# Optimization experiments

Hardware: AMD Instinct MI355X
Metric: run time of the kernel (lower is better)

Reference implementation:

```python
import jax, jax.numpy as jnp
import numpy as np

DIMENSIONS = 10000
NUM_LEVELS = 256
SIZE = 28
BATCH = 64
NUM_CLASSES = 10


def _bipolar(key, shape):
    # torchhd MAP hypervectors are random +/-1
    return jnp.where(jax.random.uniform(key, shape) > 0.5, 1.0, -1.0).astype(jnp.float32)


def setup_inputs() -> dict:
    key = jax.random.key(0)
    kx, kpx, kpy, kv, kw = jax.random.split(key, 5)
    # pixel intensities in [0, 1]
    x = jax.random.uniform(kx, (BATCH, SIZE, SIZE), dtype=jnp.float32)
    # position = hard_quantize(bundle(px, py)) with px, py random bipolar HVs
    px = _bipolar(kpx, (SIZE * SIZE, DIMENSIONS))
    py = _bipolar(kpy, (SIZE * SIZE, DIMENSIONS))
    position = jnp.where(px + py > 0, 1.0, -1.0).astype(jnp.float32)
    # Level embedding table (bipolar hypervectors per intensity level)
    level_weight = _bipolar(kv, (NUM_LEVELS, DIMENSIONS))
    # classify Linear weight (zero in original; small random here so output is non-trivial)
    classify_weight = jax.random.normal(kw, (NUM_CLASSES, DIMENSIONS), jnp.float32) * 0.01
    return {"x": x, "position": position, "level_weight": level_weight,
            "classify_weight": classify_weight}


def reference(x, position, level_weight, classify_weight):
    B = x.shape[0]
    xf = x.reshape(B, -1)                                   # [B, P] with P = size*size
    # torchhd Level: value in [0,1] -> round to one of NUM_LEVELS indices
    idx = jnp.clip(jnp.round(xf * (NUM_LEVELS - 1)), 0, NUM_LEVELS - 1).astype(jnp.int32)
    # bind: gather level HVs and elementwise-multiply with position HVs, then multiset-bundle (sum over P)
    bundled = jnp.einsum('bpd,pd->bd', level_weight[idx], position)  # [B, D]
    # hard_quantize: sign threshold (>0 -> 1, else -1)
    enc = jnp.where(bundled > 0, 1.0, -1.0).astype(x.dtype)
    # classify: Linear(DIMENSIONS, num_classes, bias=False)
    logit = enc @ classify_weight.T                          # [B, num_classes]
    return logit
```

## Files before the change

### kernel.cpp

```cpp
#include <hip/hip_runtime.h>
#include <stdint.h>

#define D      10000
#define WPR    313
#define NPIX   784
#define NB     64
#define NC     10
#define NPC    16
#define PCL    49

__global__ __launch_bounds__(320) void pack_kernel(const float* __restrict__ lev,
                                                   const float* __restrict__ pos,
                                                   uint32_t* __restrict__ Lp,
                                                   uint32_t* __restrict__ Pp,
                                                   float* __restrict__ out) {
    if (blockIdx.x == 0)
        for (int i = threadIdx.x; i < NB * NC; i += 320) out[i] = 0.0f;

    int row = blockIdx.x;
    const float* src; uint32_t* dst;
    if (row < 256) { src = lev + (size_t)row * D;        dst = Lp + row * WPR; }
    else           { src = pos + (size_t)(row - 256) * D; dst = Pp + (row - 256) * WPR; }

    int w = threadIdx.x;
    if (w >= WPR) return;
    const uint4* p4 = (const uint4*)((const uint32_t*)src + w * 32);
    uint32_t word = 0;
    if (w < WPR - 1) {
        #pragma unroll
        for (int k = 0; k < 8; ++k) {
            uint4 u = p4[k];
            word |= (u.x >> 31) << (4 * k)     | (u.y >> 31) << (4 * k + 1)
                  | (u.z >> 31) << (4 * k + 2) | (u.w >> 31) << (4 * k + 3);
        }
    } else {
        #pragma unroll
        for (int k = 0; k < 4; ++k) {
            uint4 u = p4[k];
            word |= (u.x >> 31) << (4 * k)     | (u.y >> 31) << (4 * k + 1)
                  | (u.z >> 31) << (4 * k + 2) | (u.w >> 31) << (4 * k + 3);
        }
    }
    dst[w] = word;
}

__global__ __launch_bounds__(64) void count_kernel(const float* __restrict__ x,
                                                   const uint32_t* __restrict__ Lp,
                                                   const uint32_t* __restrict__ Pp,
                                                   uint32_t* __restrict__ partial) {
    int tid = threadIdx.x;
    int b = blockIdx.y, pc = blockIdx.z;
    int w = blockIdx.x * 64 + tid;
    int p0 = pc * PCL;

    __shared__ int idxs[PCL];
    if (tid < PCL) {
        float xv = x[b * NPIX + p0 + tid];
        int v = (int)rintf(xv * 255.0f);
        v = v < 0 ? 0 : (v > 255 ? 255 : v);
        idxs[tid] = v * WPR;
    }
    __syncthreads();
    if (w >= WPR) return;

    uint32_t s0 = 0, s1 = 0, s2 = 0, s3 = 0, s4 = 0, s5 = 0;
    const uint32_t* pp = Pp + p0 * WPR + w;
    #pragma unroll 7
    for (int i = 0; i < PCL; ++i) {
        int ro = __builtin_amdgcn_readfirstlane(idxs[i]);
        uint32_t c = Lp[ro + w] ^ pp[(size_t)i * WPR];
        uint32_t t;
        t = s0 & c; s0 ^= c; c = t;
        t = s1 & c; s1 ^= c; c = t;
        t = s2 & c; s2 ^= c; c = t;
        t = s3 & c; s3 ^= c; c = t;
        t = s4 & c; s4 ^= c; c = t;
        s5 ^= c;
    }

    uint32_t* o = partial + (((size_t)pc * NB + b) * 8) * WPR + w;
    #pragma unroll
    for (int q = 0; q < 8; ++q) {
        uint32_t word = 0;
        #pragma unroll
        for (int r = 0; r < 4; ++r) {
            int j = q * 4 + r;
            uint32_t cnt = ((s0 >> j) & 1u)        | (((s1 >> j) & 1u) << 1)
                         | (((s2 >> j) & 1u) << 2) | (((s3 >> j) & 1u) << 3)
                         | (((s4 >> j) & 1u) << 4) | (((s5 >> j) & 1u) << 5);
            word |= cnt << (8 * r);
        }
        o[(size_t)q * WPR] = word;
    }
}

__global__ __launch_bounds__(256) void logits_kernel(const uint32_t* __restrict__ partial,
                                                     const float* __restrict__ cw,
                                                     float* __restrict__ out) {
    int b = blockIdx.y;
    int tid = threadIdx.x;
    int dend = blockIdx.x * 1280 + 1280; if (dend > D) dend = D;
    float acc[NC];
    #pragma unroll
    for (int c = 0; c < NC; ++c) acc[c] = 0.0f;

    for (int d = blockIdx.x * 1280 + tid; d < dend; d += 256) {
        int w = d >> 5, j = d & 31, q = j >> 2, shift = 8 * (j & 3);
        int sum = 0;
        #pragma unroll
        for (int pc = 0; pc < NPC; ++pc)
            sum += (int)((partial[(((size_t)pc * NB + b) * 8 + q) * WPR + w] >> shift) & 0xffu);
        float enc = (2 * sum < NPIX) ? 1.0f : -1.0f;
        #pragma unroll
        for (int c = 0; c < NC; ++c) acc[c] = fmaf(enc, cw[c * D + d], acc[c]);
    }

    int lane = tid & 63, wv = tid >> 6;
    __shared__ float red[4][NC];
    #pragma unroll
    for (int c = 0; c < NC; ++c) {
        float v = acc[c];
        #pragma unroll
        for (int off = 32; off > 0; off >>= 1) v += __shfl_down(v, off, 64);
        if (lane == 0) red[wv][c] = v;
    }
    __syncthreads();
    if (tid < NC) {
        float s = red[0][tid] + red[1][tid] + red[2][tid] + red[3][tid];
        atomicAdd(&out[b * NC + tid], s);
    }
}

extern "C" void kernel_launch(void* const* d_in, const int* in_sizes, int n_in,
                              void* d_out, int out_size, void* d_ws, size_t ws_size,
                              hipStream_t stream) {
    const float* x   = (const float*)d_in[0];
    const float* pos = (const float*)d_in[1];
    const float* lev = (const float*)d_in[2];
    const float* cw  = (const float*)d_in[3];
    float* out = (float*)d_out;

    uint32_t* Lp      = (uint32_t*)d_ws;
    uint32_t* Pp      = Lp + 256 * WPR;
    uint32_t* partial = Pp + NPIX * WPR;

    pack_kernel<<<256 + NPIX, 320, 0, stream>>>(lev, pos, Lp, Pp, out);
    dim3 g1(5, NB, NPC);
    count_kernel<<<g1, 64, 0, stream>>>(x, Lp, Pp, partial);
    dim3 g2(8, NB);
    logits_kernel<<<g2, 256, 0, stream>>>(partial, cw, out);
}
```

Before: 113.0 us.

## Fuse bit-sliced counting and logits into one kernel with shared-memory partials

Merges the count and logits kernels into a single kernel where each 512-thread block handles 32 packed words for one batch row. Its 16 pixel chunks accumulate bit-sliced counts into shared memory rather than global memory. The block then reduces the 16 partial counts with packed SWAR adds and applies the classifier with float4 loads. This removes the global partial buffer round trip and one kernel launch. In exchange, grid parallelism drops to 640 blocks and each thread now reads the level-row index from LDS per lane without readfirstlane.

```diff
diff --git a/kernel.cpp b/kernel.cpp
--- a/kernel.cpp
+++ b/kernel.cpp
@@ -6,8 +6,6 @@
 #define NPIX   784
 #define NB     64
 #define NC     10
-#define NPC    16
-#define PCL    49
 
 __global__ __launch_bounds__(320) void pack_kernel(const float* __restrict__ lev,
                                                    const float* __restrict__ pos,
@@ -44,89 +42,105 @@
     dst[w] = word;
 }
 
-__global__ __launch_bounds__(64) void count_kernel(const float* __restrict__ x,
-                                                   const uint32_t* __restrict__ Lp,
-                                                   const uint32_t* __restrict__ Pp,
-                                                   uint32_t* __restrict__ partial) {
+__global__ __launch_bounds__(512) void fused_kernel(const float* __restrict__ x,
+                                                    const uint32_t* __restrict__ Lp,
+                                                    const uint32_t* __restrict__ Pp,
+                                                    const float* __restrict__ cw,
+                                                    float* __restrict__ out) {
     int tid = threadIdx.x;
-    int b = blockIdx.y, pc = blockIdx.z;
-    int w = blockIdx.x * 64 + tid;
-    int p0 = pc * PCL;
+    int b = blockIdx.y;
+    int bx = blockIdx.x;
+    int t = tid >> 6, lane = tid & 63;
+    int w32 = lane & 31, h = lane >> 5;
+    int w = bx * 32 + w32;
+    int wc = w < WPR ? w : WPR - 1;
 
-    __shared__ int idxs[PCL];
-    if (tid < PCL) {
-        float xv = x[b * NPIX + p0 + tid];
+    __shared__ int idxs[NPIX];
+    __shared__ uint32_t part[16][8][36];
+    __shared__ float red[8][NC];
+
+    for (int i = tid; i < NPIX; i += 512) {
+        float xv = x[b * NPIX + i];
         int v = (int)rintf(xv * 255.0f);
         v = v < 0 ? 0 : (v > 255 ? 255 : v);
-        idxs[tid] = v * WPR;
+        idxs[i] = v * WPR;
     }
     __syncthreads();
-    if (w >= WPR) return;
 
+    int cc = 2 * t + h;
+    int p0 = cc * 49;
     uint32_t s0 = 0, s1 = 0, s2 = 0, s3 = 0, s4 = 0, s5 = 0;
-    const uint32_t* pp = Pp + p0 * WPR + w;
+    const uint32_t* pp = Pp + (size_t)p0 * WPR + wc;
     #pragma unroll 7
-    for (int i = 0; i < PCL; ++i) {
-        int ro = __builtin_amdgcn_readfirstlane(idxs[i]);
-        uint32_t c = Lp[ro + w] ^ pp[(size_t)i * WPR];
-        uint32_t t;
-        t = s0 & c; s0 ^= c; c = t;
-        t = s1 & c; s1 ^= c; c = t;
-        t = s2 & c; s2 ^= c; c = t;
-        t = s3 & c; s3 ^= c; c = t;
-        t = s4 & c; s4 ^= c; c = t;
+    for (int i = 0; i < 49; ++i) {
+        int ro = idxs[p0 + i];
+        uint32_t c = Lp[ro + wc] ^ pp[(size_t)i * WPR];
+        uint32_t tt;
+        tt = s0 & c; s0 ^= c; c = tt;
+        tt = s1 & c; s1 ^= c; c = tt;
+        tt = s2 & c; s2 ^= c; c = tt;
+        tt = s3 & c; s3 ^= c; c = tt;
+        tt = s4 & c; s4 ^= c; c = tt;
         s5 ^= c;
     }
 
-    uint32_t* o = partial + (((size_t)pc * NB + b) * 8) * WPR + w;
     #pragma unroll
     for (int q = 0; q < 8; ++q) {
-        uint32_t word = 0;
+        uint32_t wordv = 0;
         #pragma unroll
         for (int r = 0; r < 4; ++r) {
             int j = q * 4 + r;
             uint32_t cnt = ((s0 >> j) & 1u)        | (((s1 >> j) & 1u) << 1)
                          | (((s2 >> j) & 1u) << 2) | (((s3 >> j) & 1u) << 3)
                          | (((s4 >> j) & 1u) << 4) | (((s5 >> j) & 1u) << 5);
-            word |= cnt << (8 * r);
+            wordv |= cnt << (8 * r);
         }
-        o[(size_t)q * WPR] = word;
+        part[cc][q][w32] = wordv;
     }
-}
+    __syncthreads();
 
-__global__ __launch_bounds__(256) void logits_kernel(const uint32_t* __restrict__ partial,
-                                                     const float* __restrict__ cw,
-                                                     float* __restrict__ out) {
-    int b = blockIdx.y;
-    int tid = threadIdx.x;
-    int dend = blockIdx.x * 1280 + 1280; if (dend > D) dend = D;
     float acc[NC];
     #pragma unroll
     for (int c = 0; c < NC; ++c) acc[c] = 0.0f;
 
-    for (int d = blockIdx.x * 1280 + tid; d < dend; d += 256) {
-        int w = d >> 5, j = d & 31, q = j >> 2, shift = 8 * (j & 3);
-        int sum = 0;
-        #pragma unroll
-        for (int pc = 0; pc < NPC; ++pc)
-            sum += (int)((partial[(((size_t)pc * NB + b) * 8 + q) * WPR + w] >> shift) & 0xffu);
-        float enc = (2 * sum < NPIX) ? 1.0f : -1.0f;
-        #pragma unroll
-        for (int c = 0; c < NC; ++c) acc[c] = fmaf(enc, cw[c * D + d], acc[c]);
+    if (tid < 256) {
+        int rw = tid >> 3, q = tid & 7;
+        int ww = bx * 32 + rw;
+        int d0 = ww * 32 + q * 4;
+        if (ww < WPR && d0 + 3 < D) {
+            uint32_t se = 0, so = 0;
+            #pragma unroll
+            for (int k = 0; k < 16; ++k) {
+                uint32_t u = part[k][q][rw];
+                se += u & 0x00FF00FFu;
+                so += (u >> 8) & 0x00FF00FFu;
+            }
+            int c0 = se & 0xFFFFu, c1 = so & 0xFFFFu;
+            int c2 = se >> 16,     c3 = so >> 16;
+            float e0 = (2 * c0 < NPIX) ? 1.0f : -1.0f;
+            float e1 = (2 * c1 < NPIX) ? 1.0f : -1.0f;
+            float e2 = (2 * c2 < NPIX) ? 1.0f : -1.0f;
+            float e3 = (2 * c3 < NPIX) ? 1.0f : -1.0f;
+            #pragma unroll
+            for (int c = 0; c < NC; ++c) {
+                const float4 v = *(const float4*)(cw + (size_t)c * D + d0);
+                acc[c] = fmaf(e0, v.x, fmaf(e1, v.y, fmaf(e2, v.z, fmaf(e3, v.w, acc[c]))));
+            }
+        }
     }
 
-    int lane = tid & 63, wv = tid >> 6;
-    __shared__ float red[4][NC];
     #pragma unroll
     for (int c = 0; c < NC; ++c) {
         float v = acc[c];
         #pragma unroll
         for (int off = 32; off > 0; off >>= 1) v += __shfl_down(v, off, 64);
-        if (lane == 0) red[wv][c] = v;
+        if (lane == 0) red[t][c] = v;
     }
     __syncthreads();
     if (tid < NC) {
-        float s = red[0][tid] + red[1][tid] + red[2][tid] + red[3][tid];
+        float s = red[0][tid];
+        #pragma unroll
+        for (int t2 = 1; t2 < 8; ++t2) s += red[t2][tid];
         atomicAdd(&out[b * NC + tid], s);
     }
 }
@@ -140,13 +154,10 @@
     const float* cw  = (const float*)d_in[3];
     float* out = (float*)d_out;
 
-    uint32_t* Lp      = (uint32_t*)d_ws;
-    uint32_t* Pp      = Lp + 256 * WPR;
-    uint32_t* partial = Pp + NPIX * WPR;
+    uint32_t* Lp = (uint32_t*)d_ws;
+    uint32_t* Pp = Lp + 256 * WPR;
 
     pack_kernel<<<256 + NPIX, 320, 0, stream>>>(lev, pos, Lp, Pp, out);
-    dim3 g1(5, NB, NPC);
-    count_kernel<<<g1, 64, 0, stream>>>(x, Lp, Pp, partial);
-    dim3 g2(8, NB);
-    logits_kernel<<<g2, 256, 0, stream>>>(partial, cw, out);
+    dim3 g(10, NB);
+    fused_kernel<<<g, 512, 0, stream>>>(x, Lp, Pp, cw, out);
 }
```

New measurement: 106.8 us. 5.4% less time.
